# Performance work log

Hardware: AMD Instinct MI355X
Metric: run time of the kernel (lower is better)

The kernel has to match this reference:

```python
import jax, jax.numpy as jnp
import numpy as np

B, L, IN_DIM, OUT_DIM = 65536, 9, 128, 64


def setup_inputs() -> dict:
    key = jax.random.key(0)
    ks = jax.random.split(key, 9)
    s1 = 1.0 / np.sqrt(2 * IN_DIM)
    s2 = 1.0 / np.sqrt(IN_DIM)
    return {
        "value": jax.random.normal(ks[0], (B, L, IN_DIM), dtype=jnp.float32),
        "key": jax.random.normal(ks[1], (B, IN_DIM), dtype=jnp.float32),
        "seq_len": jax.random.randint(ks[2], (B,), 0, 8, dtype=jnp.int64),
        "maxlen": 9,
        # get_w: Linear(2*in_dim, in_dim) -> ReLU -> Linear(in_dim, 1)
        "w1": jax.random.uniform(ks[3], (IN_DIM, 2 * IN_DIM), jnp.float32, -s1, s1),
        "b1": jax.random.uniform(ks[4], (IN_DIM,), jnp.float32, -s1, s1),
        "w2": jax.random.uniform(ks[5], (1, IN_DIM), jnp.float32, -s2, s2),
        "b2": jax.random.uniform(ks[6], (1,), jnp.float32, -s2, s2),
        # fc: Linear(in_dim, out_dim) -> ReLU
        "fcw": jax.random.uniform(ks[7], (OUT_DIM, IN_DIM), jnp.float32, -s2, s2),
        "fcb": jax.random.uniform(ks[8], (OUT_DIM,), jnp.float32, -s2, s2),
    }


def reference(value, key, seq_len, maxlen, w1, b1, w2, b2, fcw, fcb):
    # value: [B, L, D]; key: [B, D]; L == maxlen
    Lv = value.shape[1]
    key_rep = jnp.broadcast_to(key[:, None, :], value.shape)          # [B, L, D]
    cat = jnp.concatenate([key_rep, value], axis=-1)                  # [B, L, 2D]
    h = jax.nn.relu(jnp.einsum("bld,hd->blh", cat, w1) + b1)          # [B, L, D]
    weight = (jnp.einsum("blh,oh->blo", h, w2) + b2)[..., 0]          # [B, L]
    # sequence_mask(seq_len + 1, maxlen): position t valid iff t+1 <= seq_len+1
    pos = jnp.arange(1, Lv + 1)                                       # [L]
    mask = pos[None, :] <= (seq_len + 1)[:, None]                     # [B, L] bool
    weight = jnp.where(mask, weight, -jnp.inf)
    attn = jax.nn.softmax(weight, axis=-1)                            # [B, L]
    out = jnp.einsum("bld,bl->bd", value, attn)                       # [B, D]
    out = jax.nn.relu(out @ fcw.T + fcb)                              # [B, out_dim]
    return out
```

## Files before the change

kernel.cpp:

```cpp
#include <hip/hip_runtime.h>
#include <hip/hip_bf16.h>

typedef __attribute__((ext_vector_type(8))) short short8;
typedef __attribute__((ext_vector_type(4))) float f32x4;

#define NW 8
#define BPW 16
#define BPB (NW * BPW)

static __device__ __forceinline__ unsigned pk_bf16(float a, float b) {
    unsigned d;
    asm("v_cvt_pk_bf16_f32 %0, %1, %2" : "=v"(d) : "v"(a), "v"(b));
    return d;
}

static __device__ __forceinline__ unsigned rne16(float x) {
    unsigned u = __float_as_uint(x);
    return (u + 0x7fffu + ((u >> 16) & 1u)) >> 16;
}
static __device__ __forceinline__ unsigned rne_bf16_pair(float x, float y) {
    return rne16(x) | (rne16(y) << 16);
}

static __device__ __forceinline__ short8 pack_frag(f32x4 a, f32x4 b) {
    union { unsigned u[4]; short8 s; } u;
    u.u[0] = pk_bf16(a.x, a.y);
    u.u[1] = pk_bf16(a.z, a.w);
    u.u[2] = pk_bf16(b.x, b.y);
    u.u[3] = pk_bf16(b.z, b.w);
    return u.s;
}

static __device__ __forceinline__ void stage_bfrags(const float* __restrict__ w,
                                                    int row_stride, int k_off, int nct,
                                                    short8* lds, int tid) {
    const int total = 4 * nct * 64;
    for (int idx = tid; idx < total; idx += NW * 64) {
        int lane = idx & 63;
        int ct = (idx >> 6) % nct;
        int kt = idx / (64 * nct);
        int n = ct * 16 + (lane & 15);
        int k = kt * 32 + (lane >> 4) * 8;
        const float* p = w + (size_t)n * row_stride + k_off + k;
        f32x4 a = *(const f32x4*)p;
        f32x4 b = *(const f32x4*)(p + 4);
        lds[idx] = pack_frag(a, b);
    }
}

static __device__ __forceinline__ void stage_bfrags_split(const float* __restrict__ w,
                                                          int row_stride, int nct,
                                                          short8* lds_hi, short8* lds_lo,
                                                          int tid) {
    const int total = 4 * nct * 64;
    for (int idx = tid; idx < total; idx += NW * 64) {
        int lane = idx & 63;
        int ct = (idx >> 6) % nct;
        int kt = idx / (64 * nct);
        int n = ct * 16 + (lane & 15);
        int k = kt * 32 + (lane >> 4) * 8;
        const float* p = w + (size_t)n * row_stride + k;
        f32x4 a = *(const f32x4*)p;
        f32x4 b = *(const f32x4*)(p + 4);
        float xs[8] = {a.x, a.y, a.z, a.w, b.x, b.y, b.z, b.w};
        union { unsigned u[4]; short8 s; } uh, ul;
#pragma unroll
        for (int q = 0; q < 4; ++q) {
            float x = xs[2 * q], y = xs[2 * q + 1];
            unsigned hx = rne16(x), hy = rne16(y);
            uh.u[q] = hx | (hy << 16);
            ul.u[q] = rne_bf16_pair(x - __uint_as_float(hx << 16),
                                    y - __uint_as_float(hy << 16));
        }
        lds_hi[idx] = uh.s;
        lds_lo[idx] = ul.s;
    }
}

__global__ __launch_bounds__(NW * 64, 2)
void mask_attn_fused(const float* __restrict__ value, const float* __restrict__ key,
                     const int* __restrict__ seq_len, const float* __restrict__ w1,
                     const float* __restrict__ b1, const float* __restrict__ w2,
                     const float* __restrict__ fcw, const float* __restrict__ fcb,
                     float* __restrict__ out, int B) {
    __shared__ short8 wlds[2048];
    __shared__ uint2 hklds[NW * 8 * 64];
    __shared__ f32x4 w2lds4[32];

    const int tid = threadIdx.x;
    const int wave = tid >> 6;
    const int lane = tid & 63;
    const int g = lane >> 4;
    const int lo = lane & 15;

    const long long b0w = (long long)blockIdx.x * BPB + (long long)wave * BPW;
    long long vb = b0w + lo; if (vb > (long long)B - 1) vb = (long long)B - 1;

    const float* ap = value + vb * (9 * 128) + g * 8;
    f32x4 raw[8];
#pragma unroll
    for (int h = 0; h < 8; ++h)
        raw[h] = *(const f32x4*)(ap + (h >> 1) * 32 + (h & 1) * 4);
    f32x4 kv[8];
    const float* kp = key + vb * 128 + g * 8;
#pragma unroll
    for (int h = 0; h < 8; ++h)
        kv[h] = *(const f32x4*)(kp + (h >> 1) * 32 + (h & 1) * 4);

    if (tid < 32) w2lds4[tid] = ((const f32x4*)w2)[tid];

    stage_bfrags(w1, 2 * 128, 0, 8, wlds, tid);
    __syncthreads();

    {
        short8 kf[4];
#pragma unroll
        for (int kt = 0; kt < 4; ++kt)
            kf[kt] = pack_frag(kv[2 * kt], kv[2 * kt + 1]);
#pragma unroll
        for (int ct = 0; ct < 8; ++ct) {
            f32x4 acc = *(const f32x4*)(b1 + ct * 16 + g * 4);
#pragma unroll
            for (int kt = 0; kt < 4; ++kt)
                acc = __builtin_amdgcn_mfma_f32_16x16x32_bf16(
                    wlds[(kt * 8 + ct) * 64 + lane], kf[kt], acc, 0, 0, 0);
            uint2 pk;
            pk.x = rne_bf16_pair(acc.x, acc.y);
            pk.y = rne_bf16_pair(acc.z, acc.w);
            hklds[wave * 512 + ct * 64 + lane] = pk;
        }
    }
    __syncthreads();

    stage_bfrags(w1, 2 * 128, 128, 8, wlds, tid);
    __syncthreads();

    const int sq = seq_len[vb];
    const uint2* hkw = hklds + wave * 512;

    float o[4][8];
#pragma unroll
    for (int kt = 0; kt < 4; ++kt)
#pragma unroll
        for (int j = 0; j < 8; ++j) o[kt][j] = 0.f;
    float s = 0.f, m = -3e38f;

#pragma unroll 1
    for (int l = 0; l < 9; ++l) {
        short8 af[4], alo[4];
#pragma unroll
        for (int kt = 0; kt < 4; ++kt) {
            f32x4 a = raw[2 * kt], b = raw[2 * kt + 1];
            af[kt] = pack_frag(a, b);
            float xs[8] = {a.x, a.y, a.z, a.w, b.x, b.y, b.z, b.w};
            union { unsigned u[4]; short8 s; } ul;
#pragma unroll
            for (int q = 0; q < 4; ++q) {
                float x = xs[2 * q], y = xs[2 * q + 1];
                unsigned hx = rne16(x), hy = rne16(y);
                ul.u[q] = pk_bf16(x - __uint_as_float(hx << 16),
                                  y - __uint_as_float(hy << 16));
            }
            alo[kt] = ul.s;
        }
        if (l + 1 < 9) {
#pragma unroll
            for (int h = 0; h < 8; ++h)
                raw[h] = *(const f32x4*)(ap + (l + 1) * 128 + (h >> 1) * 32 + (h & 1) * 4);
        }

        float pA = 0.f, pB = 0.f;
#pragma unroll
        for (int ct = 0; ct < 8; ++ct) {
            uint2 hkv = hkw[ct * 64 + lane];
            f32x4 acc;
            acc.x = __uint_as_float(hkv.x << 16);
            acc.y = __uint_as_float(hkv.x & 0xffff0000u);
            acc.z = __uint_as_float(hkv.y << 16);
            acc.w = __uint_as_float(hkv.y & 0xffff0000u);
#pragma unroll
            for (int kt = 0; kt < 4; ++kt)
                acc = __builtin_amdgcn_mfma_f32_16x16x32_bf16(
                    wlds[(kt * 8 + ct) * 64 + lane], af[kt], acc, 0, 0, 0);
            f32x4 wv = w2lds4[ct * 4 + g];
            if (ct & 1) {
                pB += fmaxf(acc.x, 0.f) * wv.x;
                pB += fmaxf(acc.y, 0.f) * wv.y;
                pB += fmaxf(acc.z, 0.f) * wv.z;
                pB += fmaxf(acc.w, 0.f) * wv.w;
            } else {
                pA += fmaxf(acc.x, 0.f) * wv.x;
                pA += fmaxf(acc.y, 0.f) * wv.y;
                pA += fmaxf(acc.z, 0.f) * wv.z;
                pA += fmaxf(acc.w, 0.f) * wv.w;
            }
        }
        float p = pA + pB;
        p += __shfl_xor(p, 16);
        p += __shfl_xor(p, 32);
        float w = p;

        bool valid = (l <= sq);
        float mn = valid ? fmaxf(m, w) : m;
        float c = __expf(m - mn);
        float e = valid ? __expf(w - mn) : 0.f;
        s = s * c + e;
        m = mn;
#pragma unroll
        for (int kt = 0; kt < 4; ++kt) {
            union { short8 v; unsigned u[4]; } uh, ul;
            uh.v = af[kt];
            ul.v = alo[kt];
#pragma unroll
            for (int q = 0; q < 4; ++q) {
                float h0 = __uint_as_float(uh.u[q] << 16);
                float h1 = __uint_as_float(uh.u[q] & 0xffff0000u);
                float l0 = __uint_as_float(ul.u[q] << 16);
                float l1 = __uint_as_float(ul.u[q] & 0xffff0000u);
                o[kt][2 * q]     = o[kt][2 * q] * c + e * (h0 + l0);
                o[kt][2 * q + 1] = o[kt][2 * q + 1] * c + e * (h1 + l1);
            }
        }
    }

    const float rs = 1.f / s;
    short8 afoh[4], afol[4];
#pragma unroll
    for (int kt = 0; kt < 4; ++kt) {
        union { unsigned u[4]; short8 v; } uh, ul;
#pragma unroll
        for (int p = 0; p < 4; ++p) {
            float x = o[kt][2 * p] * rs, y = o[kt][2 * p + 1] * rs;
            unsigned hx = rne16(x), hy = rne16(y);
            uh.u[p] = hx | (hy << 16);
            ul.u[p] = rne_bf16_pair(x - __uint_as_float(hx << 16),
                                    y - __uint_as_float(hy << 16));
        }
        afoh[kt] = uh.v;
        afol[kt] = ul.v;
    }

    __syncthreads();
    stage_bfrags_split(fcw, 128, 4, wlds, wlds + 1024, tid);
    __syncthreads();

    {
        f32x4 facc[4];
#pragma unroll
        for (int ct = 0; ct < 4; ++ct) {
            float fb = fcb[ct * 16 + lo];
            facc[ct] = (f32x4){fb, fb, fb, fb};
        }
#pragma unroll
        for (int kt = 0; kt < 4; ++kt)
#pragma unroll
            for (int ct = 0; ct < 4; ++ct) {
                short8 wh = wlds[(kt * 4 + ct) * 64 + lane];
                short8 wl = wlds[1024 + (kt * 4 + ct) * 64 + lane];
                facc[ct] = __builtin_amdgcn_mfma_f32_16x16x32_bf16(afoh[kt], wh, facc[ct], 0, 0, 0);
                facc[ct] = __builtin_amdgcn_mfma_f32_16x16x32_bf16(afol[kt], wh, facc[ct], 0, 0, 0);
                facc[ct] = __builtin_amdgcn_mfma_f32_16x16x32_bf16(afoh[kt], wl, facc[ct], 0, 0, 0);
            }
#pragma unroll
        for (int ct = 0; ct < 4; ++ct) {
            float v0 = fmaxf(facc[ct].x, 0.f), v1 = fmaxf(facc[ct].y, 0.f);
            float v2 = fmaxf(facc[ct].z, 0.f), v3 = fmaxf(facc[ct].w, 0.f);
            long long bo = b0w + g * 4;
            if (bo + 0 < B) out[(bo + 0) * 64 + ct * 16 + lo] = v0;
            if (bo + 1 < B) out[(bo + 1) * 64 + ct * 16 + lo] = v1;
            if (bo + 2 < B) out[(bo + 2) * 64 + ct * 16 + lo] = v2;
            if (bo + 3 < B) out[(bo + 3) * 64 + ct * 16 + lo] = v3;
        }
    }
}

extern "C" void kernel_launch(void* const* d_in, const int* in_sizes, int n_in,
                              void* d_out, int out_size, void* d_ws, size_t ws_size,
                              hipStream_t stream) {
    const float* value = (const float*)d_in[0];
    const float* key   = (const float*)d_in[1];
    const int*   seq   = (const int*)d_in[2];
    const float* w1    = (const float*)d_in[4];
    const float* b1    = (const float*)d_in[5];
    const float* w2    = (const float*)d_in[6];
    const float* fcw   = (const float*)d_in[8];
    const float* fcb   = (const float*)d_in[9];
    float* out = (float*)d_out;

    int B = in_sizes[1] / 128;
    int blocks = (B + BPB - 1) / BPB;
    mask_attn_fused<<<blocks, NW * 64, 0, stream>>>(value, key, seq, w1, b1, w2, fcw, fcb, out, B);
}
```

Baseline: 89.02 us.

## Double-buffer value rows two steps ahead and drop bf16 low-part residual in accumulation

```diff
diff --git a/kernel.cpp b/kernel.cpp
--- a/kernel.cpp
+++ b/kernel.cpp
@@ -77,6 +77,72 @@
     }
 }
 
+static __device__ __forceinline__ void stepv(int l, int lnext, const float* ap,
+                                             f32x4 (&raw)[8], const short8* wlds,
+                                             const uint2* hkw, const f32x4* w2lds4,
+                                             int lane, int g, int sq,
+                                             float& m, float& s, float (&o)[4][8]) {
+    short8 af[4];
+#pragma unroll
+    for (int kt = 0; kt < 4; ++kt)
+        af[kt] = pack_frag(raw[2 * kt], raw[2 * kt + 1]);
+    if (lnext < 9) {
+#pragma unroll
+        for (int h = 0; h < 8; ++h)
+            raw[h] = *(const f32x4*)(ap + lnext * 128 + (h >> 1) * 32 + (h & 1) * 4);
+    }
+
+    float pA = 0.f, pB = 0.f;
+#pragma unroll
+    for (int ct = 0; ct < 8; ++ct) {
+        uint2 hkv = hkw[ct * 64 + lane];
+        f32x4 acc;
+        acc.x = __uint_as_float(hkv.x << 16);
+        acc.y = __uint_as_float(hkv.x & 0xffff0000u);
+        acc.z = __uint_as_float(hkv.y << 16);
+        acc.w = __uint_as_float(hkv.y & 0xffff0000u);
+#pragma unroll
+        for (int kt = 0; kt < 4; ++kt)
+            acc = __builtin_amdgcn_mfma_f32_16x16x32_bf16(
+                wlds[(kt * 8 + ct) * 64 + lane], af[kt], acc, 0, 0, 0);
+        f32x4 wv = w2lds4[ct * 4 + g];
+        if (ct & 1) {
+            pB += fmaxf(acc.x, 0.f) * wv.x;
+            pB += fmaxf(acc.y, 0.f) * wv.y;
+            pB += fmaxf(acc.z, 0.f) * wv.z;
+            pB += fmaxf(acc.w, 0.f) * wv.w;
+        } else {
+            pA += fmaxf(acc.x, 0.f) * wv.x;
+            pA += fmaxf(acc.y, 0.f) * wv.y;
+            pA += fmaxf(acc.z, 0.f) * wv.z;
+            pA += fmaxf(acc.w, 0.f) * wv.w;
+        }
+    }
+    float p = pA + pB;
+    p += __shfl_xor(p, 16);
+    p += __shfl_xor(p, 32);
+    float w = p;
+
+    bool valid = (l <= sq);
+    float mn = valid ? fmaxf(m, w) : m;
+    float c = __expf(m - mn);
+    float e = valid ? __expf(w - mn) : 0.f;
+    s = s * c + e;
+    m = mn;
+#pragma unroll
+    for (int kt = 0; kt < 4; ++kt) {
+        union { short8 v; unsigned u[4]; } uh;
+        uh.v = af[kt];
+#pragma unroll
+        for (int q = 0; q < 4; ++q) {
+            float h0 = __uint_as_float(uh.u[q] << 16);
+            float h1 = __uint_as_float(uh.u[q] & 0xffff0000u);
+            o[kt][2 * q]     = o[kt][2 * q] * c + e * h0;
+            o[kt][2 * q + 1] = o[kt][2 * q + 1] * c + e * h1;
+        }
+    }
+}
+
 __global__ __launch_bounds__(NW * 64, 2)
 void mask_attn_fused(const float* __restrict__ value, const float* __restrict__ key,
                      const int* __restrict__ seq_len, const float* __restrict__ w1,
@@ -97,10 +163,13 @@
     long long vb = b0w + lo; if (vb > (long long)B - 1) vb = (long long)B - 1;
 
     const float* ap = value + vb * (9 * 128) + g * 8;
-    f32x4 raw[8];
+    f32x4 rawA[8], rawB[8];
 #pragma unroll
     for (int h = 0; h < 8; ++h)
-        raw[h] = *(const f32x4*)(ap + (h >> 1) * 32 + (h & 1) * 4);
+        rawA[h] = *(const f32x4*)(ap + (h >> 1) * 32 + (h & 1) * 4);
+#pragma unroll
+    for (int h = 0; h < 8; ++h)
+        rawB[h] = *(const f32x4*)(ap + 128 + (h >> 1) * 32 + (h & 1) * 4);
     f32x4 kv[8];
     const float* kp = key + vb * 128 + g * 8;
 #pragma unroll
@@ -146,81 +215,10 @@
     float s = 0.f, m = -3e38f;
 
 #pragma unroll 1
-    for (int l = 0; l < 9; ++l) {
-        short8 af[4], alo[4];
-#pragma unroll
-        for (int kt = 0; kt < 4; ++kt) {
-            f32x4 a = raw[2 * kt], b = raw[2 * kt + 1];
-            af[kt] = pack_frag(a, b);
-            float xs[8] = {a.x, a.y, a.z, a.w, b.x, b.y, b.z, b.w};
-            union { unsigned u[4]; short8 s; } ul;
-#pragma unroll
-            for (int q = 0; q < 4; ++q) {
-                float x = xs[2 * q], y = xs[2 * q + 1];
-                unsigned hx = rne16(x), hy = rne16(y);
-                ul.u[q] = pk_bf16(x - __uint_as_float(hx << 16),
-                                  y - __uint_as_float(hy << 16));
-            }
-            alo[kt] = ul.s;
-        }
-        if (l + 1 < 9) {
-#pragma unroll
-            for (int h = 0; h < 8; ++h)
-                raw[h] = *(const f32x4*)(ap + (l + 1) * 128 + (h >> 1) * 32 + (h & 1) * 4);
-        }
-
-        float pA = 0.f, pB = 0.f;
-#pragma unroll
-        for (int ct = 0; ct < 8; ++ct) {
-            uint2 hkv = hkw[ct * 64 + lane];
-            f32x4 acc;
-            acc.x = __uint_as_float(hkv.x << 16);
-            acc.y = __uint_as_float(hkv.x & 0xffff0000u);
-            acc.z = __uint_as_float(hkv.y << 16);
-            acc.w = __uint_as_float(hkv.y & 0xffff0000u);
-#pragma unroll
-            for (int kt = 0; kt < 4; ++kt)
-                acc = __builtin_amdgcn_mfma_f32_16x16x32_bf16(
-                    wlds[(kt * 8 + ct) * 64 + lane], af[kt], acc, 0, 0, 0);
-            f32x4 wv = w2lds4[ct * 4 + g];
-            if (ct & 1) {
-                pB += fmaxf(acc.x, 0.f) * wv.x;
-                pB += fmaxf(acc.y, 0.f) * wv.y;
-                pB += fmaxf(acc.z, 0.f) * wv.z;
-                pB += fmaxf(acc.w, 0.f) * wv.w;
-            } else {
-                pA += fmaxf(acc.x, 0.f) * wv.x;
-                pA += fmaxf(acc.y, 0.f) * wv.y;
-                pA += fmaxf(acc.z, 0.f) * wv.z;
-                pA += fmaxf(acc.w, 0.f) * wv.w;
-            }
-        }
-        float p = pA + pB;
-        p += __shfl_xor(p, 16);
-        p += __shfl_xor(p, 32);
-        float w = p;
-
-        bool valid = (l <= sq);
-        float mn = valid ? fmaxf(m, w) : m;
-        float c = __expf(m - mn);
-        float e = valid ? __expf(w - mn) : 0.f;
-        s = s * c + e;
-        m = mn;
-#pragma unroll
-        for (int kt = 0; kt < 4; ++kt) {
-            union { short8 v; unsigned u[4]; } uh, ul;
-            uh.v = af[kt];
-            ul.v = alo[kt];
-#pragma unroll
-            for (int q = 0; q < 4; ++q) {
-                float h0 = __uint_as_float(uh.u[q] << 16);
-                float h1 = __uint_as_float(uh.u[q] & 0xffff0000u);
-                float l0 = __uint_as_float(ul.u[q] << 16);
-                float l1 = __uint_as_float(ul.u[q] & 0xffff0000u);
-                o[kt][2 * q]     = o[kt][2 * q] * c + e * (h0 + l0);
-                o[kt][2 * q + 1] = o[kt][2 * q + 1] * c + e * (h1 + l1);
-            }
-        }
+    for (int l = 0; l < 9; l += 2) {
+        stepv(l, l + 2, ap, rawA, wlds, hkw, w2lds4, lane, g, sq, m, s, o);
+        if (l + 1 < 9)
+            stepv(l + 1, l + 3, ap, rawB, wlds, hkw, w2lds4, lane, g, sq, m, s, o);
     }
 
     const float rs = 1.f / s;
```

New measurement: 330.9 us. +271.7%, slower.
